# Optimization experiments

Hardware: AMD Instinct MI355X
Metric: run time of the kernel (lower is better)

Reference implementation:

```python
import jax, jax.numpy as jnp
import numpy as np

K, D, O, B = 65536, 256, 256, 1024

def setup_inputs() -> dict:
    key = jax.random.key(0)
    k1, k2, k3 = jax.random.split(key, 3)
    return {
        "x": jax.random.normal(k1, (B, D), dtype=jnp.float32),
        "mean": jax.random.normal(k2, (K, D), dtype=jnp.float32),
        "stddev": jnp.ones((K, D), dtype=jnp.float32),
        "outputs": jax.random.normal(k3, (K, O), dtype=jnp.float32),
        "top_k": 32,
    }

def reference(x, mean, stddev, outputs, top_k):
    # Joint Gaussian log-prob summed over feature dim, computed without the
    # [B, K, D] broadcast torch materializes. Expanding sum_d ((x-mu)/sigma)^2
    # gives three GEMM-shaped terms.
    d = x.shape[-1]
    inv_var = 1.0 / (stddev * stddev)                      # [K, D]
    quad = ((x * x) @ inv_var.T                            # [B, K]
            - 2.0 * (x @ (mean * inv_var).T)
            + jnp.sum(mean * mean * inv_var, axis=-1))
    log_norm = jnp.sum(jnp.log(stddev), axis=-1) + 0.5 * d * jnp.log(2.0 * jnp.pi)
    joint_lp = -0.5 * quad - log_norm                      # [B, K]
    top_lp, top_idx = jax.lax.top_k(joint_lp, top_k)       # [B, top_k]
    weights = jax.nn.softmax(top_lp, axis=-1)              # [B, top_k]
    gathered = outputs[top_idx]                            # [B, top_k, O]
    return jnp.einsum('bko,bk->bo', gathered, weights)     # [B, O]
```

## Files before the change

kernel.cpp:

```cpp
#include <hip/hip_runtime.h>
#include <stdint.h>

#define KCOMP 65536
#define DDIM  256
#define ODIM  256
#define BROWS 1024
#define NCB   512
#define NBLK  512
#define LOG2PI_TERM 235.2482645f

typedef float f32x4 __attribute__((ext_vector_type(4)));
typedef __bf16 bf16x8 __attribute__((ext_vector_type(8)));
typedef unsigned int u32;
typedef unsigned long long u64;
typedef unsigned short u16;

typedef __attribute__((address_space(1))) const u32 gconst_u32;
typedef __attribute__((address_space(3))) u32 lds_u32;

__device__ __forceinline__ u16 f2bf(float f) {
  u32 b = __float_as_uint(f);
  b += 0x7FFFu + ((b >> 16) & 1u);
  return (u16)(b >> 16);
}
__device__ __forceinline__ u32 fkey(float f) {
  u32 b = __float_as_uint(f);
  return b ^ ((b >> 31) ? 0xFFFFFFFFu : 0x80000000u);
}

#define DPP_ROR1 0x121
#define DPP_ROR2 0x122
#define DPP_ROR4 0x124
#define DPP_ROR8 0x128

#define WS_A     0
#define WS_KEY   (1u << 20)

__global__ void prep_A(const float* __restrict__ x, u16* __restrict__ A) {
  int l = threadIdx.x & 63;
  int wv = threadIdx.x >> 6;
  int t = blockIdx.x;
  int row = t * 16 + (l & 15);
  for (int u = 0; u < 4; ++u) {
    int cc = wv * 4 + u;
    int d0 = cc * 16 + ((l >> 4) << 2);
    float4 xv = *(const float4*)(x + (size_t)row * DDIM + d0);
    float xs[4] = {xv.x, xv.y, xv.z, xv.w};
    uint4 v;
    u32 wds[4];
    for (int e = 0; e < 4; ++e)
      wds[e] = (u32)f2bf(xs[e] * xs[e]) | ((u32)f2bf(-2.0f * xs[e]) << 16);
    v.x = wds[0]; v.y = wds[1]; v.z = wds[2]; v.w = wds[3];
    *(uint4*)(A + ((size_t)(t * 16 + cc) * 64 + l) * 8) = v;
  }
}

__global__ __launch_bounds__(256, 2)
void main_gemm(const u16* __restrict__ A_ws, const float* __restrict__ mean,
               const float* __restrict__ stdd, u32* __restrict__ ckey) {
  __shared__ __align__(16) char lds_raw[66560];
  __shared__ u32 wsel[2][32][9];
  int tid = threadIdx.x, l = tid & 63, w = tid >> 6;
  int nb = blockIdx.x;
  int g0 = nb * 8 + w * 2;
  int p = l & 15, q = l >> 4;

  bf16x8 wf[2][16];
  float myc[2];
  {
    u32* scr = (u32*)(lds_raw + w * 16640);
#pragma unroll
    for (int gs = 0; gs < 2; ++gs) {
      int comp = (g0 + gs) * 16 + p;
      const float* mrow = mean + (size_t)comp * DDIM + q * 64;
      const float* srow = stdd + (size_t)comp * DDIM + q * 64;
      float gsum = 0.f;
#pragma unroll
      for (int i = 0; i < 16; ++i) {
        float4 m4 = *(const float4*)(mrow + 4 * i);
        float4 s4 = *(const float4*)(srow + 4 * i);
        float ms[4] = {m4.x, m4.y, m4.z, m4.w};
        float ss[4] = {s4.x, s4.y, s4.z, s4.w};
        u32 wd[4];
#pragma unroll
        for (int e = 0; e < 4; ++e) {
          float iv = __builtin_amdgcn_rcpf(ss[e] * ss[e]);
          float miv = ms[e] * iv;
          wd[e] = (u32)f2bf(iv) | ((u32)f2bf(miv) << 16);
          gsum -= 0.5f * ms[e] * miv + __logf(ss[e]);
        }
        uint4 v; v.x = wd[0]; v.y = wd[1]; v.z = wd[2]; v.w = wd[3];
        *(uint4*)(scr + p * 260 + q * 64 + i * 4) = v;
      }
      gsum += __shfl_xor(gsum, 16);
      gsum += __shfl_xor(gsum, 32);
      myc[gs] = gsum - LOG2PI_TERM;
#pragma unroll
      for (int cc = 0; cc < 16; ++cc)
        wf[gs][cc] = *(const bf16x8*)(scr + p * 260 + cc * 16 + q * 4);
    }
  }
  __syncthreads();

  u32 cA = (u32)(w * 32 + p);
  u32 cB = cA + 16;
#define ASHP(B, CELL) (lds_raw + ((size_t)(B) * 32 + (CELL)) * 1024)

#define ISSUE(S, B)                                                           \
  {                                                                           \
    _Pragma("unroll")                                                         \
    for (int u = 0; u < 8; ++u) {                                             \
      int cell = w * 8 + u;                                                   \
      const u16* gsrc = A_ws +                                                \
        ((size_t)((S) * 2 + (cell >> 4)) * 16 + (cell & 15)) * 512            \
        + (size_t)l * 8;                                                      \
      __builtin_amdgcn_global_load_lds((gconst_u32*)gsrc,                     \
          (lds_u32*)ASHP(B, cell), 16, 0, 0);                                 \
    }                                                                         \
  }

#define MERGE_EMIT(ST, B)                                                     \
  {                                                                           \
    int r = tid;                                                              \
    u32 top[4] = {~0u, ~0u, ~0u, ~0u};                                        \
    _Pragma("unroll")                                                         \
    for (int j = 0; j < 8; ++j) {                                             \
      u32 key = wsel[B][r][j];                                                \
      if (key < top[3]) {                                                     \
        top[3] = key;                                                         \
        for (int z = 3; z > 0 && top[z] < top[z - 1]; --z) {                  \
          u32 tt = top[z]; top[z] = top[z - 1]; top[z - 1] = tt;              \
        }                                                                     \
      }                                                                       \
    }                                                                         \
    int rowg = (ST) * 32 + r;                                                 \
    uint4 ov; ov.x = ~top[0]; ov.y = ~top[1]; ov.z = ~top[2]; ov.w = ~top[3]; \
    *(uint4*)&ckey[((size_t)rowg * NCB + nb) * 4] = ov;                       \
  }

  ISSUE(0, 0)
  for (int s = 0; s < 32; ++s) {
    int pb = s & 1;
    __syncthreads();
    if (s < 31) ISSUE(s + 1, pb ^ 1)
    if (s > 0 && tid < 32) MERGE_EMIT(s - 1, pb ^ 1)

    f32x4 ac[2][2];
#pragma unroll
    for (int t = 0; t < 2; ++t) {
      ac[t][0] = (f32x4){0.f, 0.f, 0.f, 0.f};
      ac[t][1] = (f32x4){0.f, 0.f, 0.f, 0.f};
    }
#pragma unroll
    for (int cc = 0; cc < 16; ++cc) {
      bf16x8 a0 = *(const bf16x8*)(ASHP(pb, cc) + (size_t)l * 16);
      bf16x8 a1 = *(const bf16x8*)(ASHP(pb, 16 + cc) + (size_t)l * 16);
      ac[0][0] = __builtin_amdgcn_mfma_f32_16x16x32_bf16(a0, wf[0][cc], ac[0][0], 0, 0, 0);
      ac[0][1] = __builtin_amdgcn_mfma_f32_16x16x32_bf16(a0, wf[1][cc], ac[0][1], 0, 0, 0);
      ac[1][0] = __builtin_amdgcn_mfma_f32_16x16x32_bf16(a1, wf[0][cc], ac[1][0], 0, 0, 0);
      ac[1][1] = __builtin_amdgcn_mfma_f32_16x16x32_bf16(a1, wf[1][cc], ac[1][1], 0, 0, 0);
    }

#pragma unroll
    for (int t = 0; t < 2; ++t)
#pragma unroll
      for (int i = 0; i < 4; ++i) {
        float sA = fmaf(ac[t][0][i], -0.5f, myc[0]);
        float sB = fmaf(ac[t][1][i], -0.5f, myc[1]);
        u32 kA = (__float_as_uint(sA) & 0xFFFFFF00u) | cA;
        u32 kB = (__float_as_uint(sB) & 0xFFFFFF00u) | cB;
        u32 m1 = kA < kB ? kA : kB;
        u32 m2 = kA < kB ? kB : kA;
#define DSTEP(CTRL)                                                           \
        {                                                                     \
          u32 o1 = (u32)__builtin_amdgcn_mov_dpp((int)m1, CTRL, 0xf, 0xf, false); \
          u32 o2 = (u32)__builtin_amdgcn_mov_dpp((int)m2, CTRL, 0xf, 0xf, false); \
          u32 lo = m1 < o1 ? m1 : o1;                                         \
          u32 hi = m1 < o1 ? o1 : m1;                                         \
          u32 mn = m2 < o2 ? m2 : o2;                                         \
          m2 = hi < mn ? hi : mn;                                             \
          m1 = lo;                                                            \
        }
        DSTEP(DPP_ROR1) DSTEP(DPP_ROR2) DSTEP(DPP_ROR4) DSTEP(DPP_ROR8)
#undef DSTEP
        int r = t * 16 + q * 4 + i;
        if (p == 0) wsel[pb][r][w * 2] = m1;
        else if (p == 1) wsel[pb][r][w * 2 + 1] = m2;
      }
  }
  __syncthreads();
  if (tid < 32) MERGE_EMIT(31, 1)
#undef ISSUE
#undef MERGE_EMIT
#undef ASHP
}

__global__ __launch_bounds__(256)
void finalize(const float* __restrict__ x, const float* __restrict__ mean,
              const float* __restrict__ stdd, const float* __restrict__ outs,
              const u32* __restrict__ ckey, float* __restrict__ out) {
  __shared__ u32 cksh[2048];
  __shared__ float xr[256];
  __shared__ float part[256];
  __shared__ int selk[64];
  __shared__ float ew[32];
  __shared__ int kf[32];
  __shared__ float invs_sh;
  int tid = threadIdx.x, l = tid & 63, v = tid >> 6;
  int row = blockIdx.x;

  for (int i = tid; i < 2048; i += 256)
    cksh[i] = ckey[(size_t)row * 2048 + i];
  xr[tid] = x[(size_t)row * DDIM + tid];
  __syncthreads();

#define REDUCE_MAX(m)                                                         \
  {                                                                           \
    u32 o;                                                                    \
    o = (u32)__builtin_amdgcn_mov_dpp((int)m, DPP_ROR1, 0xf, 0xf, false);     \
    m = m > o ? m : o;                                                        \
    o = (u32)__builtin_amdgcn_mov_dpp((int)m, DPP_ROR2, 0xf, 0xf, false);     \
    m = m > o ? m : o;                                                        \
    o = (u32)__builtin_amdgcn_mov_dpp((int)m, DPP_ROR4, 0xf, 0xf, false);     \
    m = m > o ? m : o;                                                        \
    o = (u32)__builtin_amdgcn_mov_dpp((int)m, DPP_ROR8, 0xf, 0xf, false);     \
    m = m > o ? m : o;                                                        \
    o = (u32)__shfl_xor((int)m, 16); m = m > o ? m : o;                       \
    o = (u32)__shfl_xor((int)m, 32); m = m > o ? m : o;                       \
  }

  {
    u32 ext[8];
#pragma unroll
    for (int i = 0; i < 8; ++i) {
      int j = v * 512 + i * 64 + l;
      ext[i] = (cksh[j] & 0xFFFFFE00u) | ((u32)l << 3) | (u32)i;
    }
#define CSW(a, b) { if (ext[a] < ext[b]) { u32 t = ext[a]; ext[a] = ext[b]; ext[b] = t; } }
    CSW(0,1) CSW(2,3) CSW(4,5) CSW(6,7)
    CSW(0,2) CSW(1,3) CSW(4,6) CSW(5,7)
    CSW(1,2) CSW(5,6)
    CSW(0,4) CSW(1,5) CSW(2,6) CSW(3,7)
    CSW(2,4) CSW(3,5)
    CSW(1,2) CSW(3,4) CSW(5,6)
#undef CSW
    for (int it = 0; it < 16; ++it) {
      u32 m = ext[0];
      REDUCE_MAX(m)
      if (m == ext[0]) {
#pragma unroll
        for (int z = 0; z < 7; ++z) ext[z] = ext[z + 1];
        ext[7] = 0;
      }
      if (l == 0) {
        int wl = (int)((m >> 3) & 63u), wi = (int)(m & 7u);
        int j = v * 512 + wi * 64 + wl;
        selk[v * 16 + it] = (int)((u32)(j >> 2) * 128u + (~cksh[j] & 0x7Fu));
      }
    }
  }
  __syncthreads();

  {
    int j = tid >> 2, qq = tid & 3;
    int k = selk[j];
    const float* mr = mean + (size_t)k * DDIM + qq * 64;
    const float* sr = stdd + (size_t)k * DDIM + qq * 64;
    float s2 = 0.f, ls = 0.f;
    for (int i = 0; i < 16; ++i) {
      float4 m4 = *(const float4*)(mr + 4 * i);
      float4 s4 = *(const float4*)(sr + 4 * i);
      float4 x4 = *(const float4*)(&xr[qq * 64 + 4 * i]);
      { float is = 1.f / s4.x; float df = (x4.x - m4.x) * is; s2 += df * df; ls += __logf(s4.x); }
      { float is = 1.f / s4.y; float df = (x4.y - m4.y) * is; s2 += df * df; ls += __logf(s4.y); }
      { float is = 1.f / s4.z; float df = (x4.z - m4.z) * is; s2 += df * df; ls += __logf(s4.z); }
      { float is = 1.f / s4.w; float df = (x4.w - m4.w) * is; s2 += df * df; ls += __logf(s4.w); }
    }
    part[tid] = -0.5f * s2 - ls;
  }
  __syncthreads();

  if (tid < 64) {
    float lp0 = part[l * 4] + part[l * 4 + 1] + part[l * 4 + 2] +
                part[l * 4 + 3] - LOG2PI_TERM;
    u32 ext = (fkey(lp0) & 0xFFFFFFC0u) | (u32)l;
    float maxlp = 0.f, ssum = 0.f;
    for (int it = 0; it < 32; ++it) {
      u32 m = ext;
      REDUCE_MAX(m)
      int j = (int)(m & 63u);
      u32 vb = m & 0xFFFFFFC0u;
      vb ^= (vb >> 31) ? 0x80000000u : 0xFFFFFFFFu;
      float lp = __uint_as_float(vb);
      if (it == 0) maxlp = lp;
      float e = __expf(lp - maxlp);
      ssum += e;
      if (l == 0) { ew[it] = e; kf[it] = selk[j]; }
      if (j == l) ext = 0;
    }
    if (l == 0) invs_sh = 1.0f / ssum;
  }
  __syncthreads();
#undef REDUCE_MAX

  {
    float a = 0.f;
    for (int i = 0; i < 32; ++i)
      a += ew[i] * outs[(size_t)kf[i] * ODIM + tid];
    out[(size_t)row * ODIM + tid] = a * invs_sh;
  }
}

extern "C" void kernel_launch(void* const* d_in, const int* in_sizes, int n_in,
                              void* d_out, int out_size, void* d_ws, size_t ws_size,
                              hipStream_t stream) {
  const float* x = (const float*)d_in[0];
  const float* mean = (const float*)d_in[1];
  const float* stdd = (const float*)d_in[2];
  const float* outs = (const float*)d_in[3];
  char* ws = (char*)d_ws;
  u16* A_ws = (u16*)(ws + WS_A);
  u32* ckey = (u32*)(ws + WS_KEY);

  prep_A<<<64, 256, 0, stream>>>(x, A_ws);
  main_gemm<<<NBLK, 256, 0, stream>>>(A_ws, mean, stdd, ckey);
  finalize<<<BROWS, 256, 0, stream>>>(x, mean, stdd, outs, ckey,
                                      (float*)d_out);
}
```

Baseline: 402.1 us.

## Transpose MFMA operands, fold scale and bias into accumulator, use in-lane top-2

The -0.5 scale is folded into the bf16 weight operand and the per-component constant is preloaded into the accumulator, so the post-GEMM fma disappears. The MFMA operands are swapped so each lane's four accumulator values belong to different components of one batch row. The top-2 reduction then runs mostly in registers, with two cross-lane shuffles instead of four DPP steps per element. This cuts the VALU and cross-lane work in the epilogue, at the cost of slightly different bf16 rounding on the scaled weights and ds_bpermute-based shuffles.

```diff
diff --git a/kernel.cpp b/kernel.cpp
--- a/kernel.cpp
+++ b/kernel.cpp
@@ -65,8 +65,16 @@
   int g0 = nb * 8 + w * 2;
   int p = l & 15, q = l >> 4;
 
+  u32 kidv[8];
+#pragma unroll
+  for (int gs = 0; gs < 2; ++gs)
+#pragma unroll
+    for (int i = 0; i < 4; ++i)
+      kidv[gs * 4 + i] = (u32)(w * 32 + gs * 16 + q * 4 + i);
+
   bf16x8 wf[2][16];
   float myc[2];
+  f32x4 mycv[2];
   {
     u32* scr = (u32*)(lds_raw + w * 16640);
 #pragma unroll
@@ -86,7 +94,7 @@
         for (int e = 0; e < 4; ++e) {
           float iv = __builtin_amdgcn_rcpf(ss[e] * ss[e]);
           float miv = ms[e] * iv;
-          wd[e] = (u32)f2bf(iv) | ((u32)f2bf(miv) << 16);
+          wd[e] = (u32)f2bf(-0.5f * iv) | ((u32)f2bf(-0.5f * miv) << 16);
           gsum -= 0.5f * ms[e] * miv + __logf(ss[e]);
         }
         uint4 v; v.x = wd[0]; v.y = wd[1]; v.z = wd[2]; v.w = wd[3];
@@ -99,11 +107,14 @@
       for (int cc = 0; cc < 16; ++cc)
         wf[gs][cc] = *(const bf16x8*)(scr + p * 260 + cc * 16 + q * 4);
     }
-  }
-  __syncthreads();
-
-  u32 cA = (u32)(w * 32 + p);
-  u32 cB = cA + 16;
+#pragma unroll
+    for (int gs = 0; gs < 2; ++gs)
+#pragma unroll
+      for (int i = 0; i < 4; ++i)
+        mycv[gs][i] = __shfl(myc[gs], q * 4 + i);
+  }
+  __syncthreads();
+
 #define ASHP(B, CELL) (lds_raw + ((size_t)(B) * 32 + (CELL)) * 1024)
 
 #define ISSUE(S, B)                                                           \
@@ -148,45 +159,58 @@
     f32x4 ac[2][2];
 #pragma unroll
     for (int t = 0; t < 2; ++t) {
-      ac[t][0] = (f32x4){0.f, 0.f, 0.f, 0.f};
-      ac[t][1] = (f32x4){0.f, 0.f, 0.f, 0.f};
+      ac[t][0] = mycv[0];
+      ac[t][1] = mycv[1];
     }
 #pragma unroll
     for (int cc = 0; cc < 16; ++cc) {
       bf16x8 a0 = *(const bf16x8*)(ASHP(pb, cc) + (size_t)l * 16);
       bf16x8 a1 = *(const bf16x8*)(ASHP(pb, 16 + cc) + (size_t)l * 16);
-      ac[0][0] = __builtin_amdgcn_mfma_f32_16x16x32_bf16(a0, wf[0][cc], ac[0][0], 0, 0, 0);
-      ac[0][1] = __builtin_amdgcn_mfma_f32_16x16x32_bf16(a0, wf[1][cc], ac[0][1], 0, 0, 0);
-      ac[1][0] = __builtin_amdgcn_mfma_f32_16x16x32_bf16(a1, wf[0][cc], ac[1][0], 0, 0, 0);
-      ac[1][1] = __builtin_amdgcn_mfma_f32_16x16x32_bf16(a1, wf[1][cc], ac[1][1], 0, 0, 0);
-    }
-
-#pragma unroll
-    for (int t = 0; t < 2; ++t)
-#pragma unroll
-      for (int i = 0; i < 4; ++i) {
-        float sA = fmaf(ac[t][0][i], -0.5f, myc[0]);
-        float sB = fmaf(ac[t][1][i], -0.5f, myc[1]);
-        u32 kA = (__float_as_uint(sA) & 0xFFFFFF00u) | cA;
-        u32 kB = (__float_as_uint(sB) & 0xFFFFFF00u) | cB;
-        u32 m1 = kA < kB ? kA : kB;
-        u32 m2 = kA < kB ? kB : kA;
-#define DSTEP(CTRL)                                                           \
-        {                                                                     \
-          u32 o1 = (u32)__builtin_amdgcn_mov_dpp((int)m1, CTRL, 0xf, 0xf, false); \
-          u32 o2 = (u32)__builtin_amdgcn_mov_dpp((int)m2, CTRL, 0xf, 0xf, false); \
-          u32 lo = m1 < o1 ? m1 : o1;                                         \
-          u32 hi = m1 < o1 ? o1 : m1;                                         \
-          u32 mn = m2 < o2 ? m2 : o2;                                         \
-          m2 = hi < mn ? hi : mn;                                             \
-          m1 = lo;                                                            \
-        }
-        DSTEP(DPP_ROR1) DSTEP(DPP_ROR2) DSTEP(DPP_ROR4) DSTEP(DPP_ROR8)
-#undef DSTEP
-        int r = t * 16 + q * 4 + i;
-        if (p == 0) wsel[pb][r][w * 2] = m1;
-        else if (p == 1) wsel[pb][r][w * 2 + 1] = m2;
-      }
+      ac[0][0] = __builtin_amdgcn_mfma_f32_16x16x32_bf16(wf[0][cc], a0, ac[0][0], 0, 0, 0);
+      ac[0][1] = __builtin_amdgcn_mfma_f32_16x16x32_bf16(wf[1][cc], a0, ac[0][1], 0, 0, 0);
+      ac[1][0] = __builtin_amdgcn_mfma_f32_16x16x32_bf16(wf[0][cc], a1, ac[1][0], 0, 0, 0);
+      ac[1][1] = __builtin_amdgcn_mfma_f32_16x16x32_bf16(wf[1][cc], a1, ac[1][1], 0, 0, 0);
+    }
+
+#define UMIN(a, b) ((a) < (b) ? (a) : (b))
+#define UMAX(a, b) ((a) < (b) ? (b) : (a))
+#pragma unroll
+    for (int t = 0; t < 2; ++t) {
+      u32 k0 = (__float_as_uint(ac[t][0][0]) & 0xFFFFFF00u) | kidv[0];
+      u32 k1 = (__float_as_uint(ac[t][0][1]) & 0xFFFFFF00u) | kidv[1];
+      u32 k2 = (__float_as_uint(ac[t][0][2]) & 0xFFFFFF00u) | kidv[2];
+      u32 k3 = (__float_as_uint(ac[t][0][3]) & 0xFFFFFF00u) | kidv[3];
+      u32 k4 = (__float_as_uint(ac[t][1][0]) & 0xFFFFFF00u) | kidv[4];
+      u32 k5 = (__float_as_uint(ac[t][1][1]) & 0xFFFFFF00u) | kidv[5];
+      u32 k6 = (__float_as_uint(ac[t][1][2]) & 0xFFFFFF00u) | kidv[6];
+      u32 k7 = (__float_as_uint(ac[t][1][3]) & 0xFFFFFF00u) | kidv[7];
+      u32 l0 = UMIN(k0, k1), h0 = UMAX(k0, k1);
+      u32 l1 = UMIN(k2, k3), h1 = UMAX(k2, k3);
+      u32 l2 = UMIN(k4, k5), h2 = UMAX(k4, k5);
+      u32 l3 = UMIN(k6, k7), h3 = UMAX(k6, k7);
+      u32 A1 = UMIN(l0, l1), A2 = UMIN(UMAX(l0, l1), UMIN(h0, h1));
+      u32 B1 = UMIN(l2, l3), B2 = UMIN(UMAX(l2, l3), UMIN(h2, h3));
+      u32 m1 = UMIN(A1, B1), m2 = UMIN(UMAX(A1, B1), UMIN(A2, B2));
+      {
+        u32 o1 = (u32)__shfl_xor((int)m1, 16);
+        u32 o2 = (u32)__shfl_xor((int)m2, 16);
+        u32 lo = UMIN(m1, o1), hi = UMAX(m1, o1), mn = UMIN(m2, o2);
+        m1 = lo; m2 = UMIN(hi, mn);
+      }
+      {
+        u32 o1 = (u32)__shfl_xor((int)m1, 32);
+        u32 o2 = (u32)__shfl_xor((int)m2, 32);
+        u32 lo = UMIN(m1, o1), hi = UMAX(m1, o1), mn = UMIN(m2, o2);
+        m1 = lo; m2 = UMIN(hi, mn);
+      }
+      if (q == 0) {
+        int r = t * 16 + p;
+        wsel[pb][r][w * 2] = m1;
+        wsel[pb][r][w * 2 + 1] = m2;
+      }
+    }
+#undef UMIN
+#undef UMAX
   }
   __syncthreads();
   if (tid < 32) MERGE_EMIT(31, 1)
```

Result: faster. 387.8 us (-3.6%).
